# Kernel optimization log

Hardware: AMD Instinct MI355X
Metric: run time of the kernel (lower is better)

## Reference

```python
import jax, jax.numpy as jnp
import numpy as np

B, T, D, H = 2, 2048, 512, 8
HD = D // H  # head_dim = 64


def setup_inputs() -> dict:
    key = jax.random.key(0)
    k1, k2, k3, k4 = jax.random.split(key, 4)
    scale = 1.0 / np.sqrt(D)
    x = jax.random.normal(k1, (B, T, D), dtype=jnp.float32)
    periods = jax.random.randint(k2, (B, H), 0, 64, dtype=jnp.int32)
    w_qkv = jax.random.normal(k3, (3 * D, D), dtype=jnp.float32) * scale
    b_qkv = jnp.zeros((3 * D,), dtype=jnp.float32)
    w_out = jax.random.normal(k4, (D, D), dtype=jnp.float32) * scale
    b_out = jnp.zeros((D,), dtype=jnp.float32)
    return {"x": x, "periods": periods, "w_qkv": w_qkv, "b_qkv": b_qkv,
            "w_out": w_out, "b_out": b_out}


def reference(x, periods, w_qkv, b_qkv, w_out, b_out):
    # qkv projection: (B,T,3D) -> (3,B,H,T,HD)
    qkv = x @ w_qkv.T + b_qkv
    qkv = qkv.reshape(B, T, 3, H, HD).transpose(2, 0, 3, 1, 4)
    q, k, v = qkv[0], qkv[1], qkv[2]

    # periodic-causal mask: valid iff j <= i and (i-j) % p == 0, p = max(period,1)
    i_idx = jnp.arange(T, dtype=jnp.int32)[:, None]   # (T,1)
    j_idx = jnp.arange(T, dtype=jnp.int32)[None, :]   # (1,T)
    diff = i_idx - j_idx                              # (T,T)
    p = jnp.maximum(periods, 1)[:, :, None, None]     # (B,H,1,1)
    valid = (diff >= 0) & ((diff % p) == 0)           # (B,H,T,T)

    scores = jnp.einsum('bhqd,bhkd->bhqk', q, k) / np.sqrt(HD)
    scores = jnp.where(valid, scores, jnp.finfo(scores.dtype).min)
    attn = jax.nn.softmax(scores, axis=-1)

    out = jnp.einsum('bhqk,bhkd->bhqd', attn, v)
    out = out.transpose(0, 2, 1, 3).reshape(B, T, D)
    return out @ w_out.T + b_out
```

## Files before the change

### kernel.cpp

```cpp
#include <hip/hip_runtime.h>
#include <math.h>

#define B_  2
#define T_  2048
#define D_  512
#define H_  8
#define HD_ 64
#define QKVS (3*D_)

typedef __bf16 bf16x8 __attribute__((ext_vector_type(8)));
typedef float  f32x4  __attribute__((ext_vector_type(4)));

__device__ inline unsigned short f2bf(float f) {
  unsigned int u = __float_as_uint(f);
  return (unsigned short)((u + 0x7FFFu + ((u >> 16) & 1u)) >> 16);
}
__device__ inline unsigned int pack2bf(float lo, float hi) {
  return (unsigned int)f2bf(lo) | ((unsigned int)f2bf(hi) << 16);
}

__global__ void cast_all(const float* __restrict__ x,
                         const float* __restrict__ wq,
                         const float* __restrict__ wo,
                         unsigned short* __restrict__ xb,
                         unsigned short* __restrict__ wqb,
                         unsigned short* __restrict__ wob) {
  const int n_x  = (B_ * T_ * D_) / 4;
  const int n_wq = (QKVS * D_) / 4;
  const int n_wo = (D_ * D_) / 4;
  int i = blockIdx.x * blockDim.x + threadIdx.x;
  const float* src; unsigned short* dst; int off;
  if (i < n_x)                    { src = x;  dst = xb;  off = i; }
  else if (i < n_x + n_wq)        { src = wq; dst = wqb; off = i - n_x; }
  else if (i < n_x + n_wq + n_wo) { src = wo; dst = wob; off = i - n_x - n_wq; }
  else return;
  float4 v = ((const float4*)src)[off];
  ushort4 o;
  o.x = f2bf(v.x); o.y = f2bf(v.y); o.z = f2bf(v.z); o.w = f2bf(v.w);
  ((ushort4*)dst)[off] = o;
}

template<int BF16OUT>
__global__ __launch_bounds__(256, 3)
void gemm_nt_bk128(const unsigned short* __restrict__ A,
                   const unsigned short* __restrict__ Bw,
                   const float* __restrict__ bias, void* __restrict__ Cv,
                   int M, int N, int K) {
  __shared__ short Asd[4][128 * 32];
  __shared__ short Bsd[4][64 * 32];

  const int tid = threadIdx.x;
  const int w   = tid >> 6;
  const int l   = tid & 63;
  const int wr  = w >> 1;
  const int wc  = w & 1;
  const int q   = l >> 4;
  const int ml  = l & 15;
  const int arow = l >> 2;
  const int kch  = (l & 3) * 8;

  const int rowbase = blockIdx.y * 128;
  const int colbase = blockIdx.x * 64;

  f32x4 acc[4][2] = {};

  for (int k0 = 0; k0 < K; k0 += 128) {
    __syncthreads();
    #pragma unroll
    for (int pnl = 0; pnl < 4; ++pnl) {
      const int kp = k0 + pnl * 32;
      #pragma unroll
      for (int s = 0; s < 2; ++s) {
        const unsigned short* g =
            A + (size_t)(rowbase + s * 64 + w * 16 + arow) * K + kp + kch;
        __builtin_amdgcn_global_load_lds(
            (const __attribute__((address_space(1))) void*)g,
            (__attribute__((address_space(3))) void*)
                &Asd[pnl][s * 2048 + w * 512], 16, 0, 0);
      }
      const unsigned short* g =
          Bw + (size_t)(colbase + w * 16 + arow) * K + kp + kch;
      __builtin_amdgcn_global_load_lds(
          (const __attribute__((address_space(1))) void*)g,
          (__attribute__((address_space(3))) void*)&Bsd[pnl][w * 512],
          16, 0, 0);
    }
    __syncthreads();

    #pragma unroll
    for (int pnl = 0; pnl < 4; ++pnl) {
      bf16x8 af[4], bfr[2];
      #pragma unroll
      for (int mi = 0; mi < 4; ++mi)
        af[mi] = *(const bf16x8*)&Asd[pnl][(wr * 64 + mi * 16 + ml) * 32 + q * 8];
      #pragma unroll
      for (int ni = 0; ni < 2; ++ni)
        bfr[ni] = *(const bf16x8*)&Bsd[pnl][(wc * 32 + ni * 16 + ml) * 32 + q * 8];
      #pragma unroll
      for (int mi = 0; mi < 4; ++mi)
        #pragma unroll
        for (int ni = 0; ni < 2; ++ni)
          acc[mi][ni] = __builtin_amdgcn_mfma_f32_16x16x32_bf16(
              af[mi], bfr[ni], acc[mi][ni], 0, 0, 0);
    }
  }

  #pragma unroll
  for (int mi = 0; mi < 4; ++mi) {
    #pragma unroll
    for (int ni = 0; ni < 2; ++ni) {
      const int col = colbase + wc * 32 + ni * 16 + ml;
      const float bv = bias[col];
      #pragma unroll
      for (int r = 0; r < 4; ++r) {
        const int row = rowbase + wr * 64 + mi * 16 + q * 4 + r;
        const float val = acc[mi][ni][r] + bv;
        if (BF16OUT)
          ((unsigned short*)Cv)[(size_t)row * N + col] = f2bf(val);
        else
          ((float*)Cv)[(size_t)row * N + col] = val;
      }
    }
  }
}

__global__ __launch_bounds__(256)
void attn_flash4(const unsigned short* __restrict__ qkv,
                 const int* __restrict__ periods,
                 unsigned short* __restrict__ ao) {
  const int bh = blockIdx.x, slot = 62 - blockIdx.y;
  int p = periods[bh]; if (p < 1) p = 1;
  const int g  = slot / p;
  const int r  = slot - g * p;
  const int L  = (T_ - 1 - r) / p + 1;
  const int q0 = g << 6;
  if (q0 >= L) return;
  const int b = bh >> 3, h = bh & 7;
  const int Lrem = L - q0;
  const int Nkb  = min(L, q0 + 64);

  const int tid  = threadIdx.x;
  const int w    = tid >> 6;
  const int lane = tid & 63;
  const int Q = lane >> 4, c = lane & 15;

  __shared__ __align__(16) unsigned short Qs[64 * 72];
  __shared__ __align__(16) unsigned short Ks[64 * 72];
  __shared__ __align__(16) unsigned short Vt[64 * 72];

  const size_t rowb = (size_t)b * T_ * QKVS + (size_t)h * HD_;

  {
    const int u = tid >> 2, ch4 = (tid & 3) * 16;
    const int t = q0 + min(u, Lrem - 1);
    const unsigned short* gq = qkv + rowb + (size_t)(r + t * p) * QKVS + ch4;
    int4 v0 = ((const int4*)gq)[0];
    int4 v1 = ((const int4*)gq)[1];
    *(int4*)&Qs[u * 72 + ch4 + 0] = v0;
    *(int4*)&Qs[u * 72 + ch4 + 8] = v1;
  }
  __syncthreads();
  bf16x8 qf[2];
  qf[0] = *(const bf16x8*)&Qs[(w * 16 + c) * 72 + Q * 8];
  qf[1] = *(const bf16x8*)&Qs[(w * 16 + c) * 72 + Q * 8 + 32];

  const int qb      = w * 16;
  const int nqw     = min(16, Lrem - qb);
  const int qglob   = q0 + qb + c;
  const int mylastk = q0 + qb + 15;

  float m_run = -3.0e38f, l_run = 0.f;
  f32x4 o[4] = {};
  const size_t kb = rowb + D_;
  const size_t vb = rowb + 2 * D_;

  const int krow = tid >> 2, koff = (tid & 3) * 16;
  const int vkey = tid & 63, vd0 = (tid >> 6) * 8;

  int4 kp0, kp1, vp0, vp1;
  {
    const int tk = min(krow, Nkb - 1);
    const int tv = min(vkey, Nkb - 1);
    const unsigned short* gk = qkv + kb + (size_t)(r + tk * p) * QKVS + koff;
    const unsigned short* gv = qkv + vb + (size_t)(r + tv * p) * QKVS;
    kp0 = ((const int4*)gk)[0];
    kp1 = ((const int4*)gk)[1];
    vp0 = *(const int4*)(gv + vd0);
    vp1 = *(const int4*)(gv + vd0 + 32);
  }

  for (int k0 = 0; k0 < Nkb; k0 += 64) {
    __syncthreads();
    {
      *(int4*)&Ks[krow * 72 + koff + 0] = kp0;
      *(int4*)&Ks[krow * 72 + koff + 8] = kp1;
      unsigned short vh0[8], vh1[8];
      *(int4*)vh0 = vp0;
      *(int4*)vh1 = vp1;
      #pragma unroll
      for (int j = 0; j < 8; ++j) {
        Vt[(vd0 + j) * 72 + vkey]      = vh0[j];
        Vt[(vd0 + 32 + j) * 72 + vkey] = vh1[j];
      }
    }
    __syncthreads();

    if (k0 + 64 < Nkb) {
      const int tk = min(k0 + 64 + krow, Nkb - 1);
      const int tv = min(k0 + 64 + vkey, Nkb - 1);
      const unsigned short* gk = qkv + kb + (size_t)(r + tk * p) * QKVS + koff;
      const unsigned short* gv = qkv + vb + (size_t)(r + tv * p) * QKVS;
      kp0 = ((const int4*)gk)[0];
      kp1 = ((const int4*)gk)[1];
      vp0 = *(const int4*)(gv + vd0);
      vp1 = *(const int4*)(gv + vd0 + 32);
    }

    if (nqw > 0 && k0 <= mylastk) {
      float pvv[16];
      float tmax = -3.0e38f;
      #pragma unroll
      for (int mt = 0; mt < 4; ++mt) {
        if (k0 + mt * 16 <= mylastk) {
          bf16x8 a0 = *(const bf16x8*)&Ks[(mt * 16 + c) * 72 + Q * 8];
          bf16x8 a1 = *(const bf16x8*)&Ks[(mt * 16 + c) * 72 + Q * 8 + 32];
          f32x4 s = {};
          s = __builtin_amdgcn_mfma_f32_16x16x32_bf16(a0, qf[0], s, 0, 0, 0);
          s = __builtin_amdgcn_mfma_f32_16x16x32_bf16(a1, qf[1], s, 0, 0, 0);
          #pragma unroll
          for (int rg = 0; rg < 4; ++rg) {
            const int kk = k0 + mt * 16 + Q * 4 + rg;
            float v = s[rg] * 0.125f;
            v = (kk <= qglob) ? v : -3.0e38f;
            pvv[mt * 4 + rg] = v;
            tmax = fmaxf(tmax, v);
          }
        } else {
          #pragma unroll
          for (int rg = 0; rg < 4; ++rg) pvv[mt * 4 + rg] = -3.0e38f;
        }
      }

      tmax = fmaxf(tmax, __shfl_xor(tmax, 16));
      tmax = fmaxf(tmax, __shfl_xor(tmax, 32));
      const float m_new = fmaxf(m_run, tmax);
      const float alpha = __expf(m_run - m_new);
      float tsum = 0.f;
      #pragma unroll
      for (int i = 0; i < 16; ++i) {
        pvv[i] = __expf(pvv[i] - m_new);
        tsum += pvv[i];
      }
      tsum += __shfl_xor(tsum, 16);
      tsum += __shfl_xor(tsum, 32);
      l_run = l_run * alpha + tsum;
      m_run = m_new;

      bf16x8 pb[2];
      const int sq2 = (Q & 1) << 1;
      #pragma unroll
      for (int kc = 0; kc < 2; ++kc) {
        unsigned int pk0[2], pk1[2];
        pk0[0] = pack2bf(pvv[kc * 8 + 0], pvv[kc * 8 + 1]);
        pk0[1] = pack2bf(pvv[kc * 8 + 2], pvv[kc * 8 + 3]);
        pk1[0] = pack2bf(pvv[kc * 8 + 4], pvv[kc * 8 + 5]);
        pk1[1] = pack2bf(pvv[kc * 8 + 6], pvv[kc * 8 + 7]);
        int dw[4];
        #pragma unroll
        for (int d = 0; d < 4; ++d) {
          const int src = ((sq2 + (d >> 1)) << 4) + c;
          const int v0 = __shfl((int)pk0[d & 1], src);
          const int v1 = __shfl((int)pk1[d & 1], src);
          dw[d] = (Q >= 2) ? v1 : v0;
        }
        int4 bi = make_int4(dw[0], dw[1], dw[2], dw[3]);
        pb[kc] = *(bf16x8*)&bi;
      }

      #pragma unroll
      for (int ch = 0; ch < 4; ++ch)
        #pragma unroll
        for (int t2 = 0; t2 < 4; ++t2) o[ch][t2] *= alpha;
      #pragma unroll
      for (int kc = 0; kc < 2; ++kc) {
        if (k0 + kc * 32 <= mylastk) {
          #pragma unroll
          for (int ch = 0; ch < 4; ++ch) {
            bf16x8 af =
                *(const bf16x8*)&Vt[(ch * 16 + c) * 72 + kc * 32 + Q * 8];
            o[ch] = __builtin_amdgcn_mfma_f32_16x16x32_bf16(af, pb[kc], o[ch],
                                                            0, 0, 0);
          }
        }
      }
    }
  }

  if (nqw > 0 && c < nqw) {
    const float invl = 1.f / l_run;
    const int tok = r + (q0 + qb + c) * p;
    unsigned int* dst =
        (unsigned int*)(ao + (size_t)(b * T_ + tok) * D_ + h * HD_);
    #pragma unroll
    for (int ch = 0; ch < 4; ++ch)
      #pragma unroll
      for (int rp = 0; rp < 2; ++rp) {
        const int dhalf = ch * 16 + Q * 4 + rp * 2;
        dst[dhalf >> 1] =
            pack2bf(o[ch][rp * 2] * invl, o[ch][rp * 2 + 1] * invl);
      }
  }
}

extern "C" void kernel_launch(void* const* d_in, const int* in_sizes, int n_in,
                              void* d_out, int out_size, void* d_ws, size_t ws_size,
                              hipStream_t stream) {
  const float* x      = (const float*)d_in[0];
  const int*   period = (const int*)  d_in[1];
  const float* w_qkv  = (const float*)d_in[2];
  const float* b_qkv  = (const float*)d_in[3];
  const float* w_out  = (const float*)d_in[4];
  const float* b_out  = (const float*)d_in[5];
  float* out = (float*)d_out;

  const int M = B_ * T_;

  char* ws = (char*)d_ws;
  unsigned short* xb   = (unsigned short*)(ws);
  unsigned short* wqb  = (unsigned short*)(ws + (size_t)M * D_ * 2);
  unsigned short* wob  = (unsigned short*)(ws + (size_t)M * D_ * 2
                                              + (size_t)QKVS * D_ * 2);
  unsigned short* qkvb = (unsigned short*)(ws + (size_t)M * D_ * 2
                                              + (size_t)QKVS * D_ * 2
                                              + (size_t)D_ * D_ * 2);
  unsigned short* aob  = xb;

  {
    const int n4 = (M * D_ + QKVS * D_ + D_ * D_) / 4;
    cast_all<<<dim3((n4 + 255) / 256), dim3(256), 0, stream>>>(
        x, w_qkv, w_out, xb, wqb, wob);
  }

  gemm_nt_bk128<1><<<dim3(QKVS / 64, M / 128), dim3(256), 0, stream>>>(
      xb, wqb, b_qkv, qkvb, M, QKVS, D_);

  attn_flash4<<<dim3(16, 63), dim3(256), 0, stream>>>(qkvb, period, aob);

  gemm_nt_bk128<0><<<dim3(D_ / 64, M / 128), dim3(256), 0, stream>>>(
      aob, wob, b_out, out, M, D_, D_);
}
```

Before: 108.3 us.

## Split attention key range across two wave groups and merge partial softmax

The attention kernel now launches 512 threads per block. Two halves of four waves each process disjoint halves of the key blocks using separate K/V shared buffers. At the end, the second half writes its partial output and running max/sum to shared memory, and the first half merges them with log-sum-exp weights before writing bf16 output. This split-K within a block shortens the serial key loop for long sequences. In exchange it adds an LDS reduction, more barriers and more shared memory, and the loop still runs max(RA) iterations with idle halves when R is odd.

Result: no change. 107.1 us, median of 2 (-1.0%).

```diff
diff --git a/kernel.cpp b/kernel.cpp
--- a/kernel.cpp
+++ b/kernel.cpp
@@ -124,7 +124,7 @@
   }
 }
 
-__global__ __launch_bounds__(256)
+__global__ __launch_bounds__(512)
 void attn_flash4(const unsigned short* __restrict__ qkv,
                  const int* __restrict__ periods,
                  unsigned short* __restrict__ ao) {
@@ -141,30 +141,30 @@
 
   const int tid  = threadIdx.x;
   const int w    = tid >> 6;
+  const int wq   = w & 3;
+  const int half = tid >> 8;
+  const int tl   = tid & 255;
   const int lane = tid & 63;
   const int Q = lane >> 4, c = lane & 15;
 
   __shared__ __align__(16) unsigned short Qs[64 * 72];
-  __shared__ __align__(16) unsigned short Ks[64 * 72];
-  __shared__ __align__(16) unsigned short Vt[64 * 72];
+  __shared__ __align__(16) unsigned short Ks[2][64 * 72];
+  __shared__ __align__(16) unsigned short Vt[2][64 * 72];
 
   const size_t rowb = (size_t)b * T_ * QKVS + (size_t)h * HD_;
 
   {
-    const int u = tid >> 2, ch4 = (tid & 3) * 16;
+    const int u = tid >> 3, ch4 = (tid & 7) * 8;
     const int t = q0 + min(u, Lrem - 1);
     const unsigned short* gq = qkv + rowb + (size_t)(r + t * p) * QKVS + ch4;
-    int4 v0 = ((const int4*)gq)[0];
-    int4 v1 = ((const int4*)gq)[1];
-    *(int4*)&Qs[u * 72 + ch4 + 0] = v0;
-    *(int4*)&Qs[u * 72 + ch4 + 8] = v1;
+    *(int4*)&Qs[u * 72 + ch4] = *(const int4*)gq;
   }
   __syncthreads();
   bf16x8 qf[2];
-  qf[0] = *(const bf16x8*)&Qs[(w * 16 + c) * 72 + Q * 8];
-  qf[1] = *(const bf16x8*)&Qs[(w * 16 + c) * 72 + Q * 8 + 32];
-
-  const int qb      = w * 16;
+  qf[0] = *(const bf16x8*)&Qs[(wq * 16 + c) * 72 + Q * 8];
+  qf[1] = *(const bf16x8*)&Qs[(wq * 16 + c) * 72 + Q * 8 + 32];
+
+  const int qb      = wq * 16;
   const int nqw     = min(16, Lrem - qb);
   const int qglob   = q0 + qb + c;
   const int mylastk = q0 + qb + 15;
@@ -174,13 +174,18 @@
   const size_t kb = rowb + D_;
   const size_t vb = rowb + 2 * D_;
 
-  const int krow = tid >> 2, koff = (tid & 3) * 16;
-  const int vkey = tid & 63, vd0 = (tid >> 6) * 8;
+  const int krow = tl >> 2, koff = (tl & 3) * 16;
+  const int vkey = tl & 63, vd0 = ((tl >> 6) & 3) * 8;
+
+  const int R     = (Nkb + 63) >> 6;
+  const int RA    = (R + 1) >> 1;
+  const int myR   = half ? (R - RA) : RA;
+  const int kbase = half ? (RA << 6) : 0;
 
   int4 kp0, kp1, vp0, vp1;
-  {
-    const int tk = min(krow, Nkb - 1);
-    const int tv = min(vkey, Nkb - 1);
+  if (myR > 0) {
+    const int tk = min(kbase + krow, Nkb - 1);
+    const int tv = min(kbase + vkey, Nkb - 1);
     const unsigned short* gk = qkv + kb + (size_t)(r + tk * p) * QKVS + koff;
     const unsigned short* gv = qkv + vb + (size_t)(r + tv * p) * QKVS;
     kp0 = ((const int4*)gk)[0];
@@ -189,23 +194,24 @@
     vp1 = *(const int4*)(gv + vd0 + 32);
   }
 
-  for (int k0 = 0; k0 < Nkb; k0 += 64) {
+  for (int rr = 0; rr < RA; ++rr) {
+    const int k0 = kbase + (rr << 6);
     __syncthreads();
-    {
-      *(int4*)&Ks[krow * 72 + koff + 0] = kp0;
-      *(int4*)&Ks[krow * 72 + koff + 8] = kp1;
+    if (rr < myR) {
+      *(int4*)&Ks[half][krow * 72 + koff + 0] = kp0;
+      *(int4*)&Ks[half][krow * 72 + koff + 8] = kp1;
       unsigned short vh0[8], vh1[8];
       *(int4*)vh0 = vp0;
       *(int4*)vh1 = vp1;
       #pragma unroll
       for (int j = 0; j < 8; ++j) {
-        Vt[(vd0 + j) * 72 + vkey]      = vh0[j];
-        Vt[(vd0 + 32 + j) * 72 + vkey] = vh1[j];
+        Vt[half][(vd0 + j) * 72 + vkey]      = vh0[j];
+        Vt[half][(vd0 + 32 + j) * 72 + vkey] = vh1[j];
       }
     }
     __syncthreads();
 
-    if (k0 + 64 < Nkb) {
+    if (rr + 1 < myR) {
       const int tk = min(k0 + 64 + krow, Nkb - 1);
       const int tv = min(k0 + 64 + vkey, Nkb - 1);
       const unsigned short* gk = qkv + kb + (size_t)(r + tk * p) * QKVS + koff;
@@ -216,14 +222,14 @@
       vp1 = *(const int4*)(gv + vd0 + 32);
     }
 
-    if (nqw > 0 && k0 <= mylastk) {
+    if (rr < myR && nqw > 0 && k0 <= mylastk) {
       float pvv[16];
       float tmax = -3.0e38f;
       #pragma unroll
       for (int mt = 0; mt < 4; ++mt) {
         if (k0 + mt * 16 <= mylastk) {
-          bf16x8 a0 = *(const bf16x8*)&Ks[(mt * 16 + c) * 72 + Q * 8];
-          bf16x8 a1 = *(const bf16x8*)&Ks[(mt * 16 + c) * 72 + Q * 8 + 32];
+          bf16x8 a0 = *(const bf16x8*)&Ks[half][(mt * 16 + c) * 72 + Q * 8];
+          bf16x8 a1 = *(const bf16x8*)&Ks[half][(mt * 16 + c) * 72 + Q * 8 + 32];
           f32x4 s = {};
           s = __builtin_amdgcn_mfma_f32_16x16x32_bf16(a0, qf[0], s, 0, 0, 0);
           s = __builtin_amdgcn_mfma_f32_16x16x32_bf16(a1, qf[1], s, 0, 0, 0);
@@ -287,7 +293,7 @@
           #pragma unroll
           for (int ch = 0; ch < 4; ++ch) {
             bf16x8 af =
-                *(const bf16x8*)&Vt[(ch * 16 + c) * 72 + kc * 32 + Q * 8];
+                *(const bf16x8*)&Vt[half][(ch * 16 + c) * 72 + kc * 32 + Q * 8];
             o[ch] = __builtin_amdgcn_mfma_f32_16x16x32_bf16(af, pb[kc], o[ch],
                                                             0, 0, 0);
           }
@@ -296,8 +302,27 @@
     }
   }
 
-  if (nqw > 0 && c < nqw) {
-    const float invl = 1.f / l_run;
+  __syncthreads();
+  float* obuf = (float*)&Ks[0][0];
+  float* mlb  = (float*)&Vt[0][0];
+  if (half && nqw > 0) {
+    float* ob = &obuf[(wq * 64 + lane) * 17];
+    #pragma unroll
+    for (int ch = 0; ch < 4; ++ch)
+      #pragma unroll
+      for (int t2 = 0; t2 < 4; ++t2) ob[ch * 4 + t2] = o[ch][t2];
+    if (Q == 0) { mlb[wq * 32 + c] = m_run; mlb[wq * 32 + 16 + c] = l_run; }
+  }
+  __syncthreads();
+
+  if (!half && nqw > 0 && c < nqw) {
+    const float mB = mlb[wq * 32 + c];
+    const float lB = mlb[wq * 32 + 16 + c];
+    const float M  = fmaxf(m_run, mB);
+    const float wA = __expf(m_run - M);
+    const float wB = __expf(mB - M);
+    const float invl = 1.f / (wA * l_run + wB * lB);
+    const float* ob = &obuf[(wq * 64 + lane) * 17];
     const int tok = r + (q0 + qb + c) * p;
     unsigned int* dst =
         (unsigned int*)(ao + (size_t)(b * T_ + tok) * D_ + h * HD_);
@@ -306,8 +331,11 @@
       #pragma unroll
       for (int rp = 0; rp < 2; ++rp) {
         const int dhalf = ch * 16 + Q * 4 + rp * 2;
-        dst[dhalf >> 1] =
-            pack2bf(o[ch][rp * 2] * invl, o[ch][rp * 2 + 1] * invl);
+        const float v0 =
+            (wA * o[ch][rp * 2]     + wB * ob[ch * 4 + rp * 2])     * invl;
+        const float v1 =
+            (wA * o[ch][rp * 2 + 1] + wB * ob[ch * 4 + rp * 2 + 1]) * invl;
+        dst[dhalf >> 1] = pack2bf(v0, v1);
       }
   }
 }
@@ -344,7 +372,7 @@
   gemm_nt_bk128<1><<<dim3(QKVS / 64, M / 128), dim3(256), 0, stream>>>(
       xb, wqb, b_qkv, qkvb, M, QKVS, D_);
 
-  attn_flash4<<<dim3(16, 63), dim3(256), 0, stream>>>(qkvb, period, aob);
+  attn_flash4<<<dim3(16, 63), dim3(512), 0, stream>>>(qkvb, period, aob);
 
   gemm_nt_bk128<0><<<dim3(D_ / 64, M / 128), dim3(256), 0, stream>>>(
       aob, wob, b_out, out, M, D_, D_);
```
